# Kernel optimization log

Measured on AMD Instinct MI355X. Metric: run time of the kernel, lower is better.

Reference implementation:

```python
import jax, jax.numpy as jnp
import numpy as np

N_NODES = 100000
N_EDGES = 1200000
F_IN = 128
HIDDEN = 64
N_CLASSES = 2


def gcn_layer(h_in, W, b, src_sl, dst_sl, norm, n):
    # GCNConv: X' = D^{-1/2} (A + I) D^{-1/2} X W + b
    h = h_in @ W                              # [N, F_out] dense projection
    msg = h[src_sl] * norm[:, None]           # gather + per-edge normalization
    return jax.ops.segment_sum(msg, dst_sl, num_segments=n) + b  # scatter-add


def _prep_edges(edge_index, n, dtype):
    # add self-loops (PyG GCNConv default) and compute symmetric norm
    loops = jnp.arange(n, dtype=edge_index.dtype)
    src_sl = jnp.concatenate([edge_index[0], loops])
    dst_sl = jnp.concatenate([edge_index[1], loops])
    deg = jax.ops.segment_sum(jnp.ones_like(dst_sl, dtype=dtype), dst_sl, num_segments=n)
    d_inv_sqrt = jnp.where(deg > 0, jax.lax.rsqrt(deg), 0.0).astype(dtype)
    norm = d_inv_sqrt[src_sl] * d_inv_sqrt[dst_sl]
    return src_sl, dst_sl, norm


def setup_inputs() -> dict:
    key = jax.random.key(0)
    k1, k2, k3, k4 = jax.random.split(key, 4)
    x = jax.random.normal(k1, (N_NODES, F_IN), dtype=jnp.float32)
    edge_index = jax.random.randint(k2, (2, N_EDGES), 0, N_NODES, dtype=jnp.int64)
    # glorot-scaled weights like PyG GCNConv defaults
    W1 = jax.random.normal(k3, (F_IN, HIDDEN), dtype=jnp.float32) * (1.0 / np.sqrt(F_IN))
    b1 = jnp.zeros((HIDDEN,), dtype=jnp.float32)
    W2 = jax.random.normal(k4, (HIDDEN, N_CLASSES), dtype=jnp.float32) * (1.0 / np.sqrt(HIDDEN))
    b2 = jnp.zeros((N_CLASSES,), dtype=jnp.float32)
    return {"x": x, "W1": W1, "b1": b1, "W2": W2, "b2": b2, "edge_index": edge_index}


def reference(x, W1, b1, W2, b2, edge_index):
    n = x.shape[0]
    src_sl, dst_sl, norm = _prep_edges(edge_index, n, x.dtype)
    h = jax.nn.relu(gcn_layer(x, W1, b1, src_sl, dst_sl, norm, n))
    out = gcn_layer(h, W2, b2, src_sl, dst_sl, norm, n)
    return jax.nn.log_softmax(out, axis=1)
```

## Files before the change

### kernel.cpp

```cpp
#include <hip/hip_runtime.h>
#include <math.h>

#define N_NODES 100000
#define N_EDGES 1200000
#define F_IN 128
#define HIDDEN 64
#define CAP 40
#define NRANGE 8
#define FILL_CHUNKS 256
#define FILL_BLOCKS (NRANGE * FILL_CHUNKS)
#define GROWS 64
#define WT_STRIDE 136

typedef unsigned short u16;
typedef __attribute__((ext_vector_type(8))) short short8v;
typedef __attribute__((ext_vector_type(4))) float float4v;

__device__ __forceinline__ u16 f2bf(float f) {
    unsigned int u = __float_as_uint(f);
    return (u16)((u + 0x7fffu + ((u >> 16) & 1u)) >> 16);
}
__device__ __forceinline__ float bf2f(u16 h) {
    return __uint_as_float((unsigned int)h << 16);
}


__global__ void zero_kernel(int* __restrict__ cnt, int n) {
    int i = blockIdx.x * blockDim.x + threadIdx.x;
    if (i < n) cnt[i] = 0;
}


__global__ __launch_bounds__(256) void fill_kernel(const int* __restrict__ src,
                                                   const int* __restrict__ dst,
                                                   int* __restrict__ cnt,
                                                   int* __restrict__ csr) {
    const int range = blockIdx.x & (NRANGE - 1);
    const int chunk = blockIdx.x >> 3;
    const int lo = range * (N_NODES / NRANGE);
    const int hi = lo + (N_NODES / NRANGE);
    const int QUADS = N_EDGES / 4;
    const int perq = (QUADS + FILL_CHUNKS - 1) / FILL_CHUNKS;
    int q0 = chunk * perq;
    int q1 = q0 + perq; if (q1 > QUADS) q1 = QUADS;
    for (int q = q0 + threadIdx.x; q < q1; q += 256) {
        int4 d4 = ((const int4*)dst)[q];
        int4 s4 = ((const int4*)src)[q];
#pragma unroll
        for (int j = 0; j < 4; ++j) {
            int d = (j == 0) ? d4.x : (j == 1) ? d4.y : (j == 2) ? d4.z : d4.w;
            if (d >= lo && d < hi) {
                int s = (j == 0) ? s4.x : (j == 1) ? s4.y : (j == 2) ? s4.z : s4.w;
                int p = atomicAdd(&cnt[d], 1);
                if (p < CAP) csr[(size_t)d * CAP + p] = s;
            }
        }
    }
}


__global__ __launch_bounds__(256) void gemm1_kernel(const float* __restrict__ x,
                                                    const float* __restrict__ W1,
                                                    const int* __restrict__ cnt,
                                                    u16* __restrict__ hn16) {
    __shared__ u16 wt[HIDDEN * WT_STRIDE];
    const int tid = threadIdx.x;
    for (int i = tid; i < F_IN * HIDDEN; i += 256) {
        int k = i >> 6, c = i & 63;
        wt[c * WT_STRIDE + k] = f2bf(W1[i]);
    }
    __syncthreads();

    const int wave = tid >> 6, lane = tid & 63;
    const int rbase = blockIdx.x * GROWS + wave * 16;
    const int arow = rbase + (lane & 15);
    const int arl = arow < N_NODES ? arow : N_NODES - 1;
    const int kslice = (lane >> 4) * 8;

    short8v a[4];
#pragma unroll
    for (int ks = 0; ks < 4; ++ks) {
        const float* xp = &x[(size_t)arl * F_IN + ks * 32 + kslice];
        float4 v0 = *(const float4*)xp;
        float4 v1 = *(const float4*)(xp + 4);
        short8v av;
        av[0] = (short)f2bf(v0.x); av[1] = (short)f2bf(v0.y);
        av[2] = (short)f2bf(v0.z); av[3] = (short)f2bf(v0.w);
        av[4] = (short)f2bf(v1.x); av[5] = (short)f2bf(v1.y);
        av[6] = (short)f2bf(v1.z); av[7] = (short)f2bf(v1.w);
        a[ks] = av;
    }

    float dd[4];
    int crow[4];
#pragma unroll
    for (int r = 0; r < 4; ++r) {
        crow[r] = rbase + (lane >> 4) * 4 + r;
        int rc = crow[r] < N_NODES ? crow[r] : N_NODES - 1;
        dd[r] = rsqrtf((float)(cnt[rc] + 1));
    }

    const int colb = lane & 15;
#pragma unroll
    for (int ct = 0; ct < 4; ++ct) {
        float4v acc = {0.f, 0.f, 0.f, 0.f};
#pragma unroll
        for (int ks = 0; ks < 4; ++ks) {
            short8v b = *(const short8v*)&wt[(ct * 16 + colb) * WT_STRIDE + ks * 32 + kslice];
            acc = __builtin_amdgcn_mfma_f32_16x16x32_bf16(a[ks], b, acc, 0, 0, 0);
        }
#pragma unroll
        for (int r = 0; r < 4; ++r) {
            if (crow[r] < N_NODES) {
                hn16[(size_t)crow[r] * HIDDEN + ct * 16 + colb] = f2bf(acc[r] * dd[r]);
            }
        }
    }
}


__global__ __launch_bounds__(256) void gather1_kernel(const u16* __restrict__ hn16,
                                                      const int* __restrict__ cnt,
                                                      const int* __restrict__ csr,
                                                      const float* __restrict__ b1,
                                                      const float* __restrict__ W2,
                                                      float* __restrict__ h2n) {
    int v = (blockIdx.x * 256 + threadIdx.x) >> 6;
    int lane = threadIdx.x & 63;
    if (v >= N_NODES) return;
    int deg = cnt[v];
    float dd = rsqrtf((float)(deg + 1));
    int n = deg > CAP ? CAP : deg;
    const int* idx = csr + (size_t)v * CAP;
    float acc = 0.f;
    int i = 0;
    for (; i + 8 <= n; i += 8) {
        int4 q0 = *(const int4*)&idx[i];
        int4 q1 = *(const int4*)&idx[i + 4];
        float a0 = bf2f(hn16[(size_t)q0.x * HIDDEN + lane]);
        float a1 = bf2f(hn16[(size_t)q0.y * HIDDEN + lane]);
        float a2 = bf2f(hn16[(size_t)q0.z * HIDDEN + lane]);
        float a3 = bf2f(hn16[(size_t)q0.w * HIDDEN + lane]);
        float a4 = bf2f(hn16[(size_t)q1.x * HIDDEN + lane]);
        float a5 = bf2f(hn16[(size_t)q1.y * HIDDEN + lane]);
        float a6 = bf2f(hn16[(size_t)q1.z * HIDDEN + lane]);
        float a7 = bf2f(hn16[(size_t)q1.w * HIDDEN + lane]);
        acc += ((a0 + a1) + (a2 + a3)) + ((a4 + a5) + (a6 + a7));
    }
    if (i + 4 <= n) {
        int4 q = *(const int4*)&idx[i];
        float a0 = bf2f(hn16[(size_t)q.x * HIDDEN + lane]);
        float a1 = bf2f(hn16[(size_t)q.y * HIDDEN + lane]);
        float a2 = bf2f(hn16[(size_t)q.z * HIDDEN + lane]);
        float a3 = bf2f(hn16[(size_t)q.w * HIDDEN + lane]);
        acc += (a0 + a1) + (a2 + a3);
        i += 4;
    }
    for (; i < n; ++i) {
        acc += bf2f(hn16[(size_t)idx[i] * HIDDEN + lane]);
    }
    float val = dd * (acc + bf2f(hn16[(size_t)v * HIDDEN + lane])) + b1[lane];
    val = fmaxf(val, 0.f);
    float2 wv = *(const float2*)&W2[lane * 2];
    float s0 = val * wv.x;
    float s1 = val * wv.y;
#pragma unroll
    for (int m = 32; m >= 1; m >>= 1) {
        s0 += __shfl_xor(s0, m, 64);
        s1 += __shfl_xor(s1, m, 64);
    }
    if (lane == 0) {
        float2 o = {dd * s0, dd * s1};
        *(float2*)&h2n[(size_t)v * 2] = o;
    }
}


__global__ void gather2_kernel(const float* __restrict__ h2n, const int* __restrict__ cnt,
                               const int* __restrict__ csr, const float* __restrict__ b2,
                               float* __restrict__ out) {
    int v = blockIdx.x * blockDim.x + threadIdx.x;
    if (v >= N_NODES) return;
    int deg = cnt[v];
    float dd = rsqrtf((float)(deg + 1));
    int n = deg > CAP ? CAP : deg;
    const int* idx = csr + (size_t)v * CAP;
    float a0 = 0.f, a1 = 0.f;
    int i = 0;
    for (; i + 8 <= n; i += 8) {
        int4 q0 = *(const int4*)&idx[i];
        int4 q1 = *(const int4*)&idx[i + 4];
        float2 h0 = *(const float2*)&h2n[(size_t)q0.x * 2];
        float2 h1 = *(const float2*)&h2n[(size_t)q0.y * 2];
        float2 h2 = *(const float2*)&h2n[(size_t)q0.z * 2];
        float2 h3 = *(const float2*)&h2n[(size_t)q0.w * 2];
        float2 h4 = *(const float2*)&h2n[(size_t)q1.x * 2];
        float2 h5 = *(const float2*)&h2n[(size_t)q1.y * 2];
        float2 h6 = *(const float2*)&h2n[(size_t)q1.z * 2];
        float2 h7 = *(const float2*)&h2n[(size_t)q1.w * 2];
        a0 += ((h0.x + h1.x) + (h2.x + h3.x)) + ((h4.x + h5.x) + (h6.x + h7.x));
        a1 += ((h0.y + h1.y) + (h2.y + h3.y)) + ((h4.y + h5.y) + (h6.y + h7.y));
    }
    if (i + 4 <= n) {
        int4 q = *(const int4*)&idx[i];
        float2 h0 = *(const float2*)&h2n[(size_t)q.x * 2];
        float2 h1 = *(const float2*)&h2n[(size_t)q.y * 2];
        float2 h2 = *(const float2*)&h2n[(size_t)q.z * 2];
        float2 h3 = *(const float2*)&h2n[(size_t)q.w * 2];
        a0 += (h0.x + h1.x) + (h2.x + h3.x);
        a1 += (h0.y + h1.y) + (h2.y + h3.y);
        i += 4;
    }
    for (; i < n; ++i) {
        float2 hv = *(const float2*)&h2n[(size_t)idx[i] * 2];
        a0 += hv.x; a1 += hv.y;
    }
    float2 hs = *(const float2*)&h2n[(size_t)v * 2];
    float v0 = dd * (a0 + hs.x) + b2[0];
    float v1 = dd * (a1 + hs.y) + b2[1];
    float m = fmaxf(v0, v1);
    float ls = m + logf(__expf(v0 - m) + __expf(v1 - m));
    float2 o = {v0 - ls, v1 - ls};
    *(float2*)&out[(size_t)v * 2] = o;
}


extern "C" void kernel_launch(void* const* d_in, const int* in_sizes, int n_in,
                              void* d_out, int out_size, void* d_ws, size_t ws_size,
                              hipStream_t stream) {
    const float* x  = (const float*)d_in[0];
    const float* W1 = (const float*)d_in[1];
    const float* b1 = (const float*)d_in[2];
    const float* W2 = (const float*)d_in[3];
    const float* b2 = (const float*)d_in[4];
    const int* edge_index = (const int*)d_in[5];
    const int* src = edge_index;
    const int* dst = edge_index + N_EDGES;
    float* out = (float*)d_out;

    char* ws = (char*)d_ws;
    size_t off = 0;
    auto alloc = [&](size_t bytes) {
        void* p = ws + off;
        off = (off + bytes + 255) & ~(size_t)255;
        return p;
    };
    int*   cnt  = (int*)alloc(N_NODES * sizeof(int));
    int*   csr  = (int*)alloc((size_t)N_NODES * CAP * sizeof(int));
    u16*   hn16 = (u16*)alloc((size_t)N_NODES * HIDDEN * sizeof(u16));
    float* h2n  = (float*)alloc((size_t)N_NODES * 2 * sizeof(float));
    (void)ws_size;

    const int B = 256;
    const int NB_N = (N_NODES + B - 1) / B;

    zero_kernel<<<NB_N, B, 0, stream>>>(cnt, N_NODES);
    fill_kernel<<<FILL_BLOCKS, B, 0, stream>>>(src, dst, cnt, csr);

    gemm1_kernel<<<(N_NODES + GROWS - 1) / GROWS, B, 0, stream>>>(x, W1, cnt, hn16);

    gather1_kernel<<<N_NODES * 64 / B, B, 0, stream>>>(hn16, cnt, csr, b1, W2, h2n);

    gather2_kernel<<<NB_N, B, 0, stream>>>(h2n, cnt, csr, b2, out);
}
```

Before: 220.3 us.

## Use 32-bit indexing, nontemporal edge loads, and memset for count reset

Replaces 64-bit size_t index arithmetic with unsigned 32-bit shifts and multiplies in the fill and gather kernels, which may cut address-computation instructions. Edge-list loads in the fill kernel become nontemporal vector loads so they do not pollute the cache. The zero-initialisation kernel is replaced with hipMemsetAsync. The 32-bit offsets rely on all index products fitting in 32 bits.

```diff
diff --git a/kernel.cpp b/kernel.cpp
--- a/kernel.cpp
+++ b/kernel.cpp
@@ -15,6 +15,7 @@
 typedef unsigned short u16;
 typedef __attribute__((ext_vector_type(8))) short short8v;
 typedef __attribute__((ext_vector_type(4))) float float4v;
+typedef __attribute__((ext_vector_type(4))) int int4v;
 
 __device__ __forceinline__ u16 f2bf(float f) {
     unsigned int u = __float_as_uint(f);
@@ -22,12 +23,6 @@
 }
 __device__ __forceinline__ float bf2f(u16 h) {
     return __uint_as_float((unsigned int)h << 16);
-}
-
-
-__global__ void zero_kernel(int* __restrict__ cnt, int n) {
-    int i = blockIdx.x * blockDim.x + threadIdx.x;
-    if (i < n) cnt[i] = 0;
 }
 
 
@@ -43,16 +38,17 @@
     const int perq = (QUADS + FILL_CHUNKS - 1) / FILL_CHUNKS;
     int q0 = chunk * perq;
     int q1 = q0 + perq; if (q1 > QUADS) q1 = QUADS;
+    const int4v* dq = (const int4v*)dst;
+    const int4v* sq = (const int4v*)src;
     for (int q = q0 + threadIdx.x; q < q1; q += 256) {
-        int4 d4 = ((const int4*)dst)[q];
-        int4 s4 = ((const int4*)src)[q];
+        int4v d4 = __builtin_nontemporal_load(&dq[q]);
+        int4v s4 = __builtin_nontemporal_load(&sq[q]);
 #pragma unroll
         for (int j = 0; j < 4; ++j) {
-            int d = (j == 0) ? d4.x : (j == 1) ? d4.y : (j == 2) ? d4.z : d4.w;
+            int d = d4[j];
             if (d >= lo && d < hi) {
-                int s = (j == 0) ? s4.x : (j == 1) ? s4.y : (j == 2) ? s4.z : s4.w;
                 int p = atomicAdd(&cnt[d], 1);
-                if (p < CAP) csr[(size_t)d * CAP + p] = s;
+                if (p < CAP) csr[(unsigned)d * CAP + p] = s4[j];
             }
         }
     }
@@ -126,40 +122,40 @@
                                                       const float* __restrict__ W2,
                                                       float* __restrict__ h2n) {
     int v = (blockIdx.x * 256 + threadIdx.x) >> 6;
-    int lane = threadIdx.x & 63;
+    unsigned lane = threadIdx.x & 63;
     if (v >= N_NODES) return;
     int deg = cnt[v];
     float dd = rsqrtf((float)(deg + 1));
     int n = deg > CAP ? CAP : deg;
-    const int* idx = csr + (size_t)v * CAP;
+    const int* idx = csr + (unsigned)v * CAP;
     float acc = 0.f;
     int i = 0;
     for (; i + 8 <= n; i += 8) {
         int4 q0 = *(const int4*)&idx[i];
         int4 q1 = *(const int4*)&idx[i + 4];
-        float a0 = bf2f(hn16[(size_t)q0.x * HIDDEN + lane]);
-        float a1 = bf2f(hn16[(size_t)q0.y * HIDDEN + lane]);
-        float a2 = bf2f(hn16[(size_t)q0.z * HIDDEN + lane]);
-        float a3 = bf2f(hn16[(size_t)q0.w * HIDDEN + lane]);
-        float a4 = bf2f(hn16[(size_t)q1.x * HIDDEN + lane]);
-        float a5 = bf2f(hn16[(size_t)q1.y * HIDDEN + lane]);
-        float a6 = bf2f(hn16[(size_t)q1.z * HIDDEN + lane]);
-        float a7 = bf2f(hn16[(size_t)q1.w * HIDDEN + lane]);
+        float a0 = bf2f(hn16[((unsigned)q0.x << 6) + lane]);
+        float a1 = bf2f(hn16[((unsigned)q0.y << 6) + lane]);
+        float a2 = bf2f(hn16[((unsigned)q0.z << 6) + lane]);
+        float a3 = bf2f(hn16[((unsigned)q0.w << 6) + lane]);
+        float a4 = bf2f(hn16[((unsigned)q1.x << 6) + lane]);
+        float a5 = bf2f(hn16[((unsigned)q1.y << 6) + lane]);
+        float a6 = bf2f(hn16[((unsigned)q1.z << 6) + lane]);
+        float a7 = bf2f(hn16[((unsigned)q1.w << 6) + lane]);
         acc += ((a0 + a1) + (a2 + a3)) + ((a4 + a5) + (a6 + a7));
     }
     if (i + 4 <= n) {
         int4 q = *(const int4*)&idx[i];
-        float a0 = bf2f(hn16[(size_t)q.x * HIDDEN + lane]);
-        float a1 = bf2f(hn16[(size_t)q.y * HIDDEN + lane]);
-        float a2 = bf2f(hn16[(size_t)q.z * HIDDEN + lane]);
-        float a3 = bf2f(hn16[(size_t)q.w * HIDDEN + lane]);
+        float a0 = bf2f(hn16[((unsigned)q.x << 6) + lane]);
+        float a1 = bf2f(hn16[((unsigned)q.y << 6) + lane]);
+        float a2 = bf2f(hn16[((unsigned)q.z << 6) + lane]);
+        float a3 = bf2f(hn16[((unsigned)q.w << 6) + lane]);
         acc += (a0 + a1) + (a2 + a3);
         i += 4;
     }
     for (; i < n; ++i) {
-        acc += bf2f(hn16[(size_t)idx[i] * HIDDEN + lane]);
-    }
-    float val = dd * (acc + bf2f(hn16[(size_t)v * HIDDEN + lane])) + b1[lane];
+        acc += bf2f(hn16[((unsigned)idx[i] << 6) + lane]);
+    }
+    float val = dd * (acc + bf2f(hn16[((unsigned)v << 6) + lane])) + b1[lane];
     val = fmaxf(val, 0.f);
     float2 wv = *(const float2*)&W2[lane * 2];
     float s0 = val * wv.x;
@@ -171,7 +167,7 @@
     }
     if (lane == 0) {
         float2 o = {dd * s0, dd * s1};
-        *(float2*)&h2n[(size_t)v * 2] = o;
+        *(float2*)&h2n[(unsigned)v * 2] = o;
     }
 }
 
@@ -184,44 +180,45 @@
     int deg = cnt[v];
     float dd = rsqrtf((float)(deg + 1));
     int n = deg > CAP ? CAP : deg;
-    const int* idx = csr + (size_t)v * CAP;
+    const int* idx = csr + (unsigned)v * CAP;
+    const float2* hp = (const float2*)h2n;
     float a0 = 0.f, a1 = 0.f;
     int i = 0;
     for (; i + 8 <= n; i += 8) {
         int4 q0 = *(const int4*)&idx[i];
         int4 q1 = *(const int4*)&idx[i + 4];
-        float2 h0 = *(const float2*)&h2n[(size_t)q0.x * 2];
-        float2 h1 = *(const float2*)&h2n[(size_t)q0.y * 2];
-        float2 h2 = *(const float2*)&h2n[(size_t)q0.z * 2];
-        float2 h3 = *(const float2*)&h2n[(size_t)q0.w * 2];
-        float2 h4 = *(const float2*)&h2n[(size_t)q1.x * 2];
-        float2 h5 = *(const float2*)&h2n[(size_t)q1.y * 2];
-        float2 h6 = *(const float2*)&h2n[(size_t)q1.z * 2];
-        float2 h7 = *(const float2*)&h2n[(size_t)q1.w * 2];
+        float2 h0 = hp[(unsigned)q0.x];
+        float2 h1 = hp[(unsigned)q0.y];
+        float2 h2 = hp[(unsigned)q0.z];
+        float2 h3 = hp[(unsigned)q0.w];
+        float2 h4 = hp[(unsigned)q1.x];
+        float2 h5 = hp[(unsigned)q1.y];
+        float2 h6 = hp[(unsigned)q1.z];
+        float2 h7 = hp[(unsigned)q1.w];
         a0 += ((h0.x + h1.x) + (h2.x + h3.x)) + ((h4.x + h5.x) + (h6.x + h7.x));
         a1 += ((h0.y + h1.y) + (h2.y + h3.y)) + ((h4.y + h5.y) + (h6.y + h7.y));
     }
     if (i + 4 <= n) {
         int4 q = *(const int4*)&idx[i];
-        float2 h0 = *(const float2*)&h2n[(size_t)q.x * 2];
-        float2 h1 = *(const float2*)&h2n[(size_t)q.y * 2];
-        float2 h2 = *(const float2*)&h2n[(size_t)q.z * 2];
-        float2 h3 = *(const float2*)&h2n[(size_t)q.w * 2];
+        float2 h0 = hp[(unsigned)q.x];
+        float2 h1 = hp[(unsigned)q.y];
+        float2 h2 = hp[(unsigned)q.z];
+        float2 h3 = hp[(unsigned)q.w];
         a0 += (h0.x + h1.x) + (h2.x + h3.x);
         a1 += (h0.y + h1.y) + (h2.y + h3.y);
         i += 4;
     }
     for (; i < n; ++i) {
-        float2 hv = *(const float2*)&h2n[(size_t)idx[i] * 2];
+        float2 hv = hp[(unsigned)idx[i]];
         a0 += hv.x; a1 += hv.y;
     }
-    float2 hs = *(const float2*)&h2n[(size_t)v * 2];
+    float2 hs = hp[(unsigned)v];
     float v0 = dd * (a0 + hs.x) + b2[0];
     float v1 = dd * (a1 + hs.y) + b2[1];
     float m = fmaxf(v0, v1);
     float ls = m + logf(__expf(v0 - m) + __expf(v1 - m));
     float2 o = {v0 - ls, v1 - ls};
-    *(float2*)&out[(size_t)v * 2] = o;
+    *(float2*)&out[(unsigned)v * 2] = o;
 }
 
 
@@ -254,7 +251,7 @@
     const int B = 256;
     const int NB_N = (N_NODES + B - 1) / B;
 
-    zero_kernel<<<NB_N, B, 0, stream>>>(cnt, N_NODES);
+    hipMemsetAsync(cnt, 0, N_NODES * sizeof(int), stream);
     fill_kernel<<<FILL_BLOCKS, B, 0, stream>>>(src, dst, cnt, csr);
 
     gemm1_kernel<<<(N_NODES + GROWS - 1) / GROWS, B, 0, stream>>>(x, W1, cnt, hn16);
```

Result: no change. 219.9 us (-0.2%).
